# Kernel optimization log

Measured on AMD Instinct MI355X. Metric: run time of the kernel, lower is better.

Reference implementation:

```python
import jax, jax.numpy as jnp
import numpy as np

N = 50000      # nodes
E = 600000     # edges
IN = 128       # in_channels
HID = 128      # GCN hidden width (fixed in module)
H = 4          # TransformerConv heads
C = 32         # out_channels per head (heads*C = 128)


def _lin(k, fan_in, fan_out):
    return jax.random.normal(k, (fan_in, fan_out), jnp.float32) / np.sqrt(fan_in)


def setup_inputs() -> dict:
    key = jax.random.key(0)
    ks = jax.random.split(key, 12)
    return {
        "x": jax.random.normal(ks[0], (N, IN), jnp.float32),
        "edge_index": jax.random.randint(ks[1], (2, E), 0, N, dtype=jnp.int32),
        "W_gcn": _lin(ks[2], IN, HID),
        "b_gcn": jnp.zeros((HID,), jnp.float32),
        "Wq": _lin(ks[3], HID, H * C),
        "bq": jnp.zeros((H * C,), jnp.float32),
        "Wk": _lin(ks[4], HID, H * C),
        "bk": jnp.zeros((H * C,), jnp.float32),
        "Wv": _lin(ks[5], HID, H * C),
        "bv": jnp.zeros((H * C,), jnp.float32),
        "Ws": _lin(ks[6], HID, H * C),
        "bs": jnp.zeros((H * C,), jnp.float32),
    }


def reference(x, edge_index, W_gcn, b_gcn, Wq, bq, Wk, bk, Wv, bv, Ws, bs):
    n = x.shape[0]
    idt = edge_index.dtype

    # ---- GCNConv: x' = D^{-1/2}(A+I)D^{-1/2} x W + b, then ReLU ----
    h = x @ W_gcn                                   # [N, HID] linear first (PyG order)
    loop = jnp.arange(n, dtype=idt)
    src = jnp.concatenate([edge_index[0], loop])    # with self-loops
    tgt = jnp.concatenate([edge_index[1], loop])
    deg = jax.ops.segment_sum(jnp.ones(src.shape, h.dtype), tgt, num_segments=n)
    dinv = jnp.where(deg > 0, jax.lax.rsqrt(deg), 0.0)
    norm = dinv[src] * dinv[tgt]                    # [E+N]
    h = jax.ops.segment_sum(h[src] * norm[:, None], tgt, num_segments=n)
    h = jax.nn.relu(h + b_gcn)                      # [N, HID]

    # ---- TransformerConv (heads=4, concat=True, no self-loops added) ----
    s, t = edge_index[0], edge_index[1]
    q = (h @ Wq + bq).reshape(n, H, C)
    k = (h @ Wk + bk).reshape(n, H, C)
    v = (h @ Wv + bv).reshape(n, H, C)

    alpha = jnp.einsum('ehc,ehc->eh', q[t], k[s]) / np.sqrt(C)   # [E, H]
    m = jax.lax.stop_gradient(jax.ops.segment_max(alpha, t, num_segments=n))
    ea = jnp.exp(alpha - m[t])
    denom = jax.ops.segment_sum(ea, t, num_segments=n)           # [N, H]
    w = ea / jnp.where(denom[t] > 0, denom[t], 1.0)              # softmax per target node

    out = jax.ops.segment_sum(w[:, :, None] * v[s], t, num_segments=n)  # [N, H, C]
    out = out.reshape(n, H * C)

    # root/skip connection (lin_skip)
    return out + h @ Ws + bs
```

## Files before the change

kernel.cpp:

```cpp
#include <hip/hip_runtime.h>
#include <hip/hip_bf16.h>

typedef __attribute__((ext_vector_type(8))) short short8;
typedef __attribute__((ext_vector_type(4))) float floatx4;
typedef _Float16 half2v __attribute__((ext_vector_type(2)));

__device__ __forceinline__ float ld_f(const void* p, int f32, int i) {
  if (f32) return ((const float*)p)[i];
  unsigned short u = ((const unsigned short*)p)[i];
  return __uint_as_float(((unsigned)u) << 16);
}
__device__ __forceinline__ short ld_bf(const void* p, int f32, int i) {
  if (!f32) return ((const short*)p)[i];
  __hip_bfloat16 h = __float2bfloat16(((const float*)p)[i]);
  return *reinterpret_cast<short*>(&h);
}
__device__ __forceinline__ unsigned short f_to_bfu(float v) {
  __hip_bfloat16 h = __float2bfloat16(v);
  return *reinterpret_cast<unsigned short*>(&h);
}
__device__ __forceinline__ short f_to_h(float v) {
  _Float16 h = (_Float16)v;
  return *reinterpret_cast<short*>(&h);
}

__global__ void init_kernel(const unsigned short* __restrict__ xs, int* __restrict__ flag,
                            int* __restrict__ cnt, int N) {
  if (blockIdx.x == 0) {
    __shared__ int sbad;
    if (threadIdx.x == 0) sbad = 0;
    __syncthreads();
    int bad = 0;
    for (int j = 2 * threadIdx.x; j < 16384; j += 512) {
      unsigned e = (xs[j] >> 7) & 0xFF;
      if (e >= 0xF0) bad = 1;
    }
    if (bad) atomicOr(&sbad, 1);
    __syncthreads();
    if (threadIdx.x == 0) flag[0] = sbad;
    return;
  }
  int i = (blockIdx.x - 1) * blockDim.x + threadIdx.x;
  if (i < N) cnt[i] = 0;
}

__global__ void prep_hist(const void* bg, const void* bq, const void* bk, const void* bv,
                          const void* bs, const void* Wg, const void* Wq, const void* Wk,
                          const void* Wv, const void* Ws, const int* __restrict__ flag,
                          float* __restrict__ bgf, float* __restrict__ bias512,
                          short* __restrict__ WpG, short* __restrict__ WpQ,
                          const int* __restrict__ ei, int* __restrict__ cnt, int E, int Gp) {
  if ((int)blockIdx.x >= Gp) {
    int e = (blockIdx.x - Gp) * blockDim.x + threadIdx.x;
    if (e < E) atomicAdd(&cnt[ei[E + e]], 1);
    return;
  }
  int tid = blockIdx.x * blockDim.x + threadIdx.x;
  int f = *flag;
  if (tid < 128) { bgf[tid] = ld_f(bg, f, tid); return; }
  if (tid < 640) {
    int t = tid - 128;
    const void* b = (t < 128) ? bq : (t < 256) ? bk : (t < 384) ? bv : bs;
    bias512[t] = ld_f(b, f, t & 127);
    return;
  }
  if (tid < 640 + 2048) {
    int id = tid - 640;
    int lane = id & 63, kb = (id >> 6) & 3, tn = id >> 8;
    int k0 = kb * 32 + (lane >> 4) * 8;
    int n = tn * 16 + (lane & 15);
    short* dst = WpG + (size_t)id * 8;
#pragma unroll
    for (int j = 0; j < 8; ++j) dst[j] = ld_bf(Wg, f, (k0 + j) * 128 + n);
    return;
  }
  if (tid < 640 + 2048 + 8192) {
    int id = tid - 640 - 2048;
    int lane = id & 63, kb = (id >> 6) & 3, tn = id >> 8;
    int k0 = kb * 32 + (lane >> 4) * 8;
    int n = tn * 16 + (lane & 15);
    const void* W = (n < 128) ? Wq : (n < 256) ? Wk : (n < 384) ? Wv : Ws;
    int col = n & 127;
    short* dst = WpQ + (size_t)id * 8;
#pragma unroll
    for (int j = 0; j < 8; ++j) dst[j] = ld_bf(W, f, (k0 + j) * 128 + col);
  }
}

__global__ void scanA(const int* __restrict__ cnt, int* __restrict__ chunkscan,
                      int* __restrict__ partials, int N) {
  __shared__ int sh[1024];
  int t = threadIdx.x;
  int g = blockIdx.x * 1024 + t;
  int v = (g < N) ? cnt[g] : 0;
  sh[t] = v;
  __syncthreads();
  for (int o = 1; o < 1024; o <<= 1) {
    int add = (t >= o) ? sh[t - o] : 0;
    __syncthreads();
    sh[t] += add;
    __syncthreads();
  }
  if (g < N) chunkscan[g] = sh[t];
  if (t == 1023) partials[blockIdx.x] = sh[1023];
}

__global__ void scanB(int* __restrict__ partials, int nb) {
  if (threadIdx.x == 0) {
    int run = 0;
    for (int b = 0; b < nb; ++b) {
      int t = partials[b];
      partials[b] = run;
      run += t;
    }
  }
}

__global__ void scanC(const int* __restrict__ cnt, const int* __restrict__ chunkscan,
                      const int* __restrict__ partials, int* __restrict__ rowptr,
                      int* __restrict__ cursor, float* __restrict__ dinv, int N) {
  int g = blockIdx.x * blockDim.x + threadIdx.x;
  if (g == 0) rowptr[0] = 0;
  if (g >= N) return;
  int c = cnt[g];
  int inc = chunkscan[g] + partials[g >> 10];
  rowptr[g + 1] = inc;
  cursor[g] = inc - c;
  dinv[g] = rsqrtf((float)c + 1.0f);
}

__global__ void gemmh0_fill(const void* __restrict__ X, const int* __restrict__ flag,
                            const short* __restrict__ Bp, const float* __restrict__ dinv,
                            short* __restrict__ C, int M, const int* __restrict__ ei,
                            int* __restrict__ cursor, int* __restrict__ srcs, int E, int Gg) {
  if ((int)blockIdx.x >= Gg) {
    int e = (blockIdx.x - Gg) * blockDim.x + threadIdx.x;
    if (e < E) {
      int t = ei[E + e];
      int pos = atomicAdd(&cursor[t], 1);
      srcs[pos] = ei[e];
    }
    return;
  }
  int wv = (blockIdx.x * blockDim.x + threadIdx.x) >> 6;
  int lane = threadIdx.x & 63;
  int tilesM = (M + 15) >> 4;
  if (wv >= tilesM) return;
  int f = *flag;
  int tm = wv;
  int m = tm * 16 + (lane & 15);
  int mc = m < M ? m : M - 1;
  int quad = lane >> 4;
  short8 a[4];
  if (f) {
    const float* xr = (const float*)X + (size_t)mc * 128 + quad * 8;
#pragma unroll
    for (int kb = 0; kb < 4; ++kb)
#pragma unroll
      for (int j = 0; j < 8; ++j) a[kb][j] = (short)f_to_bfu(xr[kb * 32 + j]);
  } else {
    const short* xr = (const short*)X + (size_t)mc * 128 + quad * 8;
#pragma unroll
    for (int kb = 0; kb < 4; ++kb) a[kb] = *(const short8*)(xr + kb * 32);
  }
  floatx4 acc[8];
#pragma unroll
  for (int tn = 0; tn < 8; ++tn) acc[tn] = (floatx4){0.f, 0.f, 0.f, 0.f};
#pragma unroll
  for (int kb = 0; kb < 4; ++kb) {
#pragma unroll
    for (int tn = 0; tn < 8; ++tn) {
      short8 b8 = *(const short8*)(Bp + ((size_t)(tn * 4 + kb) * 64 + lane) * 8);
      acc[tn] = __builtin_amdgcn_mfma_f32_16x16x32_bf16(a[kb], b8, acc[tn], 0, 0, 0);
    }
  }
  int row0 = tm * 16 + quad * 4;
  int cl = lane & 15;
  float dsc[4];
#pragma unroll
  for (int r = 0; r < 4; ++r) dsc[r] = (row0 + r < M) ? dinv[row0 + r] : 0.f;
#pragma unroll
  for (int tn = 0; tn < 8; ++tn)
#pragma unroll
    for (int r = 0; r < 4; ++r)
      if (row0 + r < M)
        C[(size_t)(row0 + r) * 128 + tn * 16 + cl] = (short)f_to_bfu(acc[tn][r] * dsc[r]);
}

__global__ void gcn_gather(const int* __restrict__ rowptr, const int* __restrict__ srcs,
                           const float* __restrict__ dinv, const unsigned* __restrict__ h0,
                           const float* __restrict__ bgf, unsigned* __restrict__ hbf, int N) {
  int node = (int)((blockIdx.x * (long long)blockDim.x + threadIdx.x) >> 6);
  if (node >= N) return;
  int lane = threadIdx.x & 63;
  int beg = rowptr[node], end = rowptr[node + 1];
  float ax = 0.f, ay = 0.f;
  int i = beg;
  for (; i + 3 < end; i += 4) {
    int s0 = srcs[i], s1 = srcs[i + 1], s2 = srcs[i + 2], s3 = srcs[i + 3];
    unsigned w0 = h0[(size_t)s0 * 64 + lane];
    unsigned w1 = h0[(size_t)s1 * 64 + lane];
    unsigned w2 = h0[(size_t)s2 * 64 + lane];
    unsigned w3 = h0[(size_t)s3 * 64 + lane];
    ax += __uint_as_float(w0 << 16) + __uint_as_float(w1 << 16) +
          __uint_as_float(w2 << 16) + __uint_as_float(w3 << 16);
    ay += __uint_as_float(w0 & 0xFFFF0000u) + __uint_as_float(w1 & 0xFFFF0000u) +
          __uint_as_float(w2 & 0xFFFF0000u) + __uint_as_float(w3 & 0xFFFF0000u);
  }
  for (; i < end; ++i) {
    unsigned w = h0[(size_t)srcs[i] * 64 + lane];
    ax += __uint_as_float(w << 16);
    ay += __uint_as_float(w & 0xFFFF0000u);
  }
  float dt = dinv[node];
  unsigned hw = h0[(size_t)node * 64 + lane];
  float2 bb = ((const float2*)bgf)[lane];
  float vx = (ax + __uint_as_float(hw << 16)) * dt + bb.x;
  float vy = (ay + __uint_as_float(hw & 0xFFFF0000u)) * dt + bb.y;
  vx = vx > 0.f ? vx : 0.f;
  vy = vy > 0.f ? vy : 0.f;
  hbf[(size_t)node * 64 + lane] = (unsigned)f_to_bfu(vx) | ((unsigned)f_to_bfu(vy) << 16);
}

__global__ void gemm_qkvs(const short* __restrict__ A, const short* __restrict__ Bp,
                          const float* __restrict__ bias512, short* __restrict__ qb,
                          short* __restrict__ kb_, short* __restrict__ vb,
                          short* __restrict__ skipb, int M) {
  int wv = (blockIdx.x * blockDim.x + threadIdx.x) >> 6;
  int lane = threadIdx.x & 63;
  int tilesM = (M + 15) >> 4;
  if (wv >= tilesM * 4) return;
  int tng = wv & 3, tm = wv >> 2;
  int m = tm * 16 + (lane & 15);
  int mc = m < M ? m : M - 1;
  int quad = lane >> 4;
  const short* Arow = A + (size_t)mc * 128 + quad * 8;
  short8 a[4];
#pragma unroll
  for (int kb = 0; kb < 4; ++kb) a[kb] = *(const short8*)(Arow + kb * 32);
  floatx4 acc[8];
#pragma unroll
  for (int j = 0; j < 8; ++j) acc[j] = (floatx4){0.f, 0.f, 0.f, 0.f};
#pragma unroll
  for (int kb = 0; kb < 4; ++kb) {
#pragma unroll
    for (int j = 0; j < 8; ++j) {
      int tn = tng * 8 + j;
      short8 b8 = *(const short8*)(Bp + ((size_t)(tn * 4 + kb) * 64 + lane) * 8);
      acc[j] = __builtin_amdgcn_mfma_f32_16x16x32_bf16(a[kb], b8, acc[j], 0, 0, 0);
    }
  }
  int row0 = tm * 16 + quad * 4;
  int cl = lane & 15;
  short* o = (tng == 0) ? qb : (tng == 1) ? kb_ : (tng == 2) ? vb : skipb;
  bool ash = tng < 2;
#pragma unroll
  for (int j = 0; j < 8; ++j) {
    int cc = j * 16 + cl;
    float b = bias512[tng * 128 + cc];
#pragma unroll
    for (int r = 0; r < 4; ++r) {
      int row = row0 + r;
      if (row >= M) continue;
      float val = acc[j][r] + b;
      o[(size_t)row * 128 + cc] = ash ? f_to_h(val) : (short)f_to_bfu(val);
    }
  }
}

__device__ __forceinline__ float dotred(half2v q2, unsigned kw) {
  half2v k2 = *reinterpret_cast<half2v*>(&kw);
#if __has_builtin(__builtin_amdgcn_fdot2)
  float p = __builtin_amdgcn_fdot2(q2, k2, 0.f, false);
#else
  float p = (float)q2[0] * (float)k2[0] + (float)q2[1] * (float)k2[1];
#endif
  p += __shfl_xor(p, 1, 16);
  p += __shfl_xor(p, 2, 16);
  p += __shfl_xor(p, 4, 16);
  p += __shfl_xor(p, 8, 16);
  return p * 0.17677669529663687f;
}

__global__ void attn_fused(const int* __restrict__ rowptr, const int* __restrict__ srcs,
                           const unsigned* __restrict__ qb, const unsigned* __restrict__ kb,
                           const unsigned* __restrict__ vb, const unsigned* __restrict__ skipb,
                           float* __restrict__ out, int N) {
  int node = (int)((blockIdx.x * (long long)blockDim.x + threadIdx.x) >> 6);
  if (node >= N) return;
  int lane = threadIdx.x & 63;
  unsigned qw = qb[(size_t)node * 64 + lane];
  half2v q2 = *reinterpret_cast<half2v*>(&qw);
  int beg = rowptr[node], end = rowptr[node + 1];

  float denom = 0.f, ax = 0.f, ay = 0.f;
  int i = beg;
  for (; i + 3 < end; i += 4) {
    int s0 = srcs[i], s1 = srcs[i + 1], s2 = srcs[i + 2], s3 = srcs[i + 3];
    unsigned kw0 = kb[(size_t)s0 * 64 + lane];
    unsigned kw1 = kb[(size_t)s1 * 64 + lane];
    unsigned kw2 = kb[(size_t)s2 * 64 + lane];
    unsigned kw3 = kb[(size_t)s3 * 64 + lane];
    unsigned vw0 = vb[(size_t)s0 * 64 + lane];
    unsigned vw1 = vb[(size_t)s1 * 64 + lane];
    unsigned vw2 = vb[(size_t)s2 * 64 + lane];
    unsigned vw3 = vb[(size_t)s3 * 64 + lane];
    float e0 = __expf(dotred(q2, kw0));
    float e1 = __expf(dotred(q2, kw1));
    float e2 = __expf(dotred(q2, kw2));
    float e3 = __expf(dotred(q2, kw3));
    denom += e0 + e1 + e2 + e3;
    ax += e0 * __uint_as_float(vw0 << 16) + e1 * __uint_as_float(vw1 << 16) +
          e2 * __uint_as_float(vw2 << 16) + e3 * __uint_as_float(vw3 << 16);
    ay += e0 * __uint_as_float(vw0 & 0xFFFF0000u) + e1 * __uint_as_float(vw1 & 0xFFFF0000u) +
          e2 * __uint_as_float(vw2 & 0xFFFF0000u) + e3 * __uint_as_float(vw3 & 0xFFFF0000u);
  }
  for (; i < end; ++i) {
    int s = srcs[i];
    unsigned kw = kb[(size_t)s * 64 + lane];
    unsigned vw = vb[(size_t)s * 64 + lane];
    float ea = __expf(dotred(q2, kw));
    denom += ea;
    ax += ea * __uint_as_float(vw << 16);
    ay += ea * __uint_as_float(vw & 0xFFFF0000u);
  }
  float r = denom > 0.f ? 1.f / denom : 0.f;
  unsigned sw = skipb[(size_t)node * 64 + lane];
  float2 o;
  o.x = ax * r + __uint_as_float(sw << 16);
  o.y = ay * r + __uint_as_float(sw & 0xFFFF0000u);
  ((float2*)out)[(size_t)node * 64 + lane] = o;
}

extern "C" void kernel_launch(void* const* d_in, const int* in_sizes, int n_in,
                              void* d_out, int out_size, void* d_ws, size_t ws_size,
                              hipStream_t stream) {
  const void* x  = d_in[0];
  const int* ei  = (const int*)d_in[1];
  const void* Wg = d_in[2];
  const void* bg = d_in[3];
  const void* Wq = d_in[4];
  const void* bq = d_in[5];
  const void* Wk = d_in[6];
  const void* bk = d_in[7];
  const void* Wv = d_in[8];
  const void* bv = d_in[9];
  const void* Ws = d_in[10];
  const void* bs = d_in[11];
  float* out = (float*)d_out;

  const int N = in_sizes[0] / 128;
  const int E = in_sizes[1] / 2;
  int tilesM = (N + 15) / 16;
  int nscan = (N + 1023) / 1024;
  const int B = 256;

  char* ws = (char*)d_ws;
  size_t off = 0;
  auto carve = [&](size_t bytes) -> void* {
    void* p = ws + off;
    off += (bytes + 255) & ~(size_t)255;
    return p;
  };
  int* flag = (int*)carve(256);
  float* bias512 = (float*)carve(512 * 4);
  float* bgf = (float*)carve(128 * 4);
  float* dinv = (float*)carve((size_t)N * 4);
  int* cnt = (int*)carve((size_t)N * 4);
  int* rowptr = (int*)carve((size_t)(N + 1) * 4);
  int* cursor = (int*)carve((size_t)N * 4);
  int* chunkscan = (int*)carve((size_t)N * 4);
  int* partials = (int*)carve((size_t)(nscan + 1) * 4);
  int* srcs = (int*)carve((size_t)E * 4);
  short* WpG = (short*)carve((size_t)16384 * 2);
  short* WpQ = (short*)carve((size_t)65536 * 2);
  short* h0bf = (short*)carve((size_t)N * 128 * 2);
  short* hbf = (short*)carve((size_t)N * 128 * 2);
  short* qb = (short*)carve((size_t)N * 128 * 2);
  short* kb = (short*)carve((size_t)N * 128 * 2);
  short* vb = (short*)carve((size_t)N * 128 * 2);
  short* skipb = (short*)carve((size_t)N * 128 * 2);

  int Gp = (10880 + B - 1) / B;
  int Gh = (E + B - 1) / B;
  int Gg = (tilesM * 64 + B - 1) / B;
  int Gf = (E + B - 1) / B;

  init_kernel<<<1 + (N + B - 1) / B, B, 0, stream>>>((const unsigned short*)x, flag, cnt, N);
  prep_hist<<<Gp + Gh, B, 0, stream>>>(bg, bq, bk, bv, bs, Wg, Wq, Wk, Wv, Ws, flag,
                                       bgf, bias512, WpG, WpQ, ei, cnt, E, Gp);
  scanA<<<nscan, 1024, 0, stream>>>(cnt, chunkscan, partials, N);
  scanB<<<1, 64, 0, stream>>>(partials, nscan);
  scanC<<<(N + B - 1) / B, B, 0, stream>>>(cnt, chunkscan, partials, rowptr, cursor, dinv, N);
  gemmh0_fill<<<Gg + Gf, B, 0, stream>>>(x, flag, WpG, dinv, h0bf, N, ei, cursor, srcs, E, Gg);
  gcn_gather<<<(N + 3) / 4, B, 0, stream>>>(rowptr, srcs, dinv, (const unsigned*)h0bf, bgf,
                                            (unsigned*)hbf, N);
  gemm_qkvs<<<(tilesM * 4 + 3) / 4, B, 0, stream>>>(hbf, WpQ, bias512, qb, kb, vb, skipb, N);
  attn_fused<<<(N + 3) / 4, B, 0, stream>>>(rowptr, srcs, (const unsigned*)qb,
                                            (const unsigned*)kb, (const unsigned*)vb,
                                            (const unsigned*)skipb, out, N);
}
```

Baseline: 298.2 us.

## Interleave K/V rows and split edges across sub-wavefronts in gather kernels

Q/K/V/skip GEMM now writes K and V into one interleaved buffer (4 fp16 K values next to 4 bf16 V values per 16-byte chunk). The attention kernel can then fetch both with a single 16-byte load per edge, and each half-wavefront handles alternate edges with a cross-half shuffle reduction at the end. The GCN gather likewise processes four edges at once per wavefront using 16-byte loads per lane, then reduces across quarters. This aims to cut the number of memory transactions per edge and improve latency hiding. The cost is extra cross-lane shuffles, and the final write is done by only part of the lanes.

```diff
diff --git a/kernel.cpp b/kernel.cpp
--- a/kernel.cpp
+++ b/kernel.cpp
@@ -23,6 +23,8 @@
   _Float16 h = (_Float16)v;
   return *reinterpret_cast<short*>(&h);
 }
+__device__ __forceinline__ float bflo(unsigned w) { return __uint_as_float(w << 16); }
+__device__ __forceinline__ float bfhi(unsigned w) { return __uint_as_float(w & 0xFFFF0000u); }
 
 __global__ void init_kernel(const unsigned short* __restrict__ xs, int* __restrict__ flag,
                             int* __restrict__ cnt, int N) {
@@ -193,39 +195,76 @@
   int node = (int)((blockIdx.x * (long long)blockDim.x + threadIdx.x) >> 6);
   if (node >= N) return;
   int lane = threadIdx.x & 63;
+  int q = lane >> 4, sl = lane & 15;
   int beg = rowptr[node], end = rowptr[node + 1];
-  float ax = 0.f, ay = 0.f;
-  int i = beg;
-  for (; i + 3 < end; i += 4) {
-    int s0 = srcs[i], s1 = srcs[i + 1], s2 = srcs[i + 2], s3 = srcs[i + 3];
-    unsigned w0 = h0[(size_t)s0 * 64 + lane];
-    unsigned w1 = h0[(size_t)s1 * 64 + lane];
-    unsigned w2 = h0[(size_t)s2 * 64 + lane];
-    unsigned w3 = h0[(size_t)s3 * 64 + lane];
-    ax += __uint_as_float(w0 << 16) + __uint_as_float(w1 << 16) +
-          __uint_as_float(w2 << 16) + __uint_as_float(w3 << 16);
-    ay += __uint_as_float(w0 & 0xFFFF0000u) + __uint_as_float(w1 & 0xFFFF0000u) +
-          __uint_as_float(w2 & 0xFFFF0000u) + __uint_as_float(w3 & 0xFFFF0000u);
-  }
-  for (; i < end; ++i) {
-    unsigned w = h0[(size_t)srcs[i] * 64 + lane];
-    ax += __uint_as_float(w << 16);
-    ay += __uint_as_float(w & 0xFFFF0000u);
-  }
-  float dt = dinv[node];
-  unsigned hw = h0[(size_t)node * 64 + lane];
-  float2 bb = ((const float2*)bgf)[lane];
-  float vx = (ax + __uint_as_float(hw << 16)) * dt + bb.x;
-  float vy = (ay + __uint_as_float(hw & 0xFFFF0000u)) * dt + bb.y;
-  vx = vx > 0.f ? vx : 0.f;
-  vy = vy > 0.f ? vy : 0.f;
-  hbf[(size_t)node * 64 + lane] = (unsigned)f_to_bfu(vx) | ((unsigned)f_to_bfu(vy) << 16);
+  float a0 = 0.f, a1 = 0.f, a2 = 0.f, a3 = 0.f, a4 = 0.f, a5 = 0.f, a6 = 0.f, a7 = 0.f;
+  int i = beg + q;
+  for (; i + 4 < end; i += 8) {
+    int s0 = srcs[i], s1 = srcs[i + 4];
+    uint4 w0 = *(const uint4*)(h0 + (size_t)s0 * 64 + sl * 4);
+    uint4 w1 = *(const uint4*)(h0 + (size_t)s1 * 64 + sl * 4);
+    a0 += bflo(w0.x) + bflo(w1.x);
+    a1 += bfhi(w0.x) + bfhi(w1.x);
+    a2 += bflo(w0.y) + bflo(w1.y);
+    a3 += bfhi(w0.y) + bfhi(w1.y);
+    a4 += bflo(w0.z) + bflo(w1.z);
+    a5 += bfhi(w0.z) + bfhi(w1.z);
+    a6 += bflo(w0.w) + bflo(w1.w);
+    a7 += bfhi(w0.w) + bfhi(w1.w);
+  }
+  if (i < end) {
+    int s0 = srcs[i];
+    uint4 w0 = *(const uint4*)(h0 + (size_t)s0 * 64 + sl * 4);
+    a0 += bflo(w0.x);
+    a1 += bfhi(w0.x);
+    a2 += bflo(w0.y);
+    a3 += bfhi(w0.y);
+    a4 += bflo(w0.z);
+    a5 += bfhi(w0.z);
+    a6 += bflo(w0.w);
+    a7 += bfhi(w0.w);
+  }
+  a0 += __shfl_xor(a0, 16); a0 += __shfl_xor(a0, 32);
+  a1 += __shfl_xor(a1, 16); a1 += __shfl_xor(a1, 32);
+  a2 += __shfl_xor(a2, 16); a2 += __shfl_xor(a2, 32);
+  a3 += __shfl_xor(a3, 16); a3 += __shfl_xor(a3, 32);
+  a4 += __shfl_xor(a4, 16); a4 += __shfl_xor(a4, 32);
+  a5 += __shfl_xor(a5, 16); a5 += __shfl_xor(a5, 32);
+  a6 += __shfl_xor(a6, 16); a6 += __shfl_xor(a6, 32);
+  a7 += __shfl_xor(a7, 16); a7 += __shfl_xor(a7, 32);
+  if (q == 0) {
+    uint4 hw = *(const uint4*)(h0 + (size_t)node * 64 + sl * 4);
+    float dt = dinv[node];
+    const float4* bb = (const float4*)bgf;
+    float4 b0 = bb[sl * 2], b1 = bb[sl * 2 + 1];
+    float v0 = (a0 + bflo(hw.x)) * dt + b0.x;
+    float v1 = (a1 + bfhi(hw.x)) * dt + b0.y;
+    float v2 = (a2 + bflo(hw.y)) * dt + b0.z;
+    float v3 = (a3 + bfhi(hw.y)) * dt + b0.w;
+    float v4 = (a4 + bflo(hw.z)) * dt + b1.x;
+    float v5 = (a5 + bfhi(hw.z)) * dt + b1.y;
+    float v6 = (a6 + bflo(hw.w)) * dt + b1.z;
+    float v7 = (a7 + bfhi(hw.w)) * dt + b1.w;
+    v0 = v0 > 0.f ? v0 : 0.f;
+    v1 = v1 > 0.f ? v1 : 0.f;
+    v2 = v2 > 0.f ? v2 : 0.f;
+    v3 = v3 > 0.f ? v3 : 0.f;
+    v4 = v4 > 0.f ? v4 : 0.f;
+    v5 = v5 > 0.f ? v5 : 0.f;
+    v6 = v6 > 0.f ? v6 : 0.f;
+    v7 = v7 > 0.f ? v7 : 0.f;
+    uint4 o;
+    o.x = (unsigned)f_to_bfu(v0) | ((unsigned)f_to_bfu(v1) << 16);
+    o.y = (unsigned)f_to_bfu(v2) | ((unsigned)f_to_bfu(v3) << 16);
+    o.z = (unsigned)f_to_bfu(v4) | ((unsigned)f_to_bfu(v5) << 16);
+    o.w = (unsigned)f_to_bfu(v6) | ((unsigned)f_to_bfu(v7) << 16);
+    *(uint4*)(hbf + (size_t)node * 64 + sl * 4) = o;
+  }
 }
 
 __global__ void gemm_qkvs(const short* __restrict__ A, const short* __restrict__ Bp,
                           const float* __restrict__ bias512, short* __restrict__ qb,
-                          short* __restrict__ kb_, short* __restrict__ vb,
-                          short* __restrict__ skipb, int M) {
+                          short* __restrict__ kvb, short* __restrict__ skipb, int M) {
   int wv = (blockIdx.x * blockDim.x + threadIdx.x) >> 6;
   int lane = threadIdx.x & 63;
   int tilesM = (M + 15) >> 4;
@@ -252,8 +291,6 @@
   }
   int row0 = tm * 16 + quad * 4;
   int cl = lane & 15;
-  short* o = (tng == 0) ? qb : (tng == 1) ? kb_ : (tng == 2) ? vb : skipb;
-  bool ash = tng < 2;
 #pragma unroll
   for (int j = 0; j < 8; ++j) {
     int cc = j * 16 + cl;
@@ -263,73 +300,88 @@
       int row = row0 + r;
       if (row >= M) continue;
       float val = acc[j][r] + b;
-      o[(size_t)row * 128 + cc] = ash ? f_to_h(val) : (short)f_to_bfu(val);
-    }
-  }
-}
-
-__device__ __forceinline__ float dotred(half2v q2, unsigned kw) {
-  half2v k2 = *reinterpret_cast<half2v*>(&kw);
+      if (tng == 0) {
+        qb[(size_t)row * 128 + cc] = f_to_h(val);
+      } else if (tng == 3) {
+        skipb[(size_t)row * 128 + cc] = (short)f_to_bfu(val);
+      } else {
+        size_t base = (size_t)row * 256 + (size_t)((cc >> 2) * 8 + (cc & 3));
+        if (tng == 1)
+          kvb[base] = f_to_h(val);
+        else
+          kvb[base + 4] = (short)f_to_bfu(val);
+      }
+    }
+  }
+}
+
+__device__ __forceinline__ float dotred8(half2v qa, half2v qc, unsigned kw0, unsigned kw1) {
+  half2v k0 = *reinterpret_cast<half2v*>(&kw0);
+  half2v k1 = *reinterpret_cast<half2v*>(&kw1);
 #if __has_builtin(__builtin_amdgcn_fdot2)
-  float p = __builtin_amdgcn_fdot2(q2, k2, 0.f, false);
+  float p = __builtin_amdgcn_fdot2(qa, k0, 0.f, false);
+  p = __builtin_amdgcn_fdot2(qc, k1, p, false);
 #else
-  float p = (float)q2[0] * (float)k2[0] + (float)q2[1] * (float)k2[1];
+  float p = (float)qa[0] * (float)k0[0] + (float)qa[1] * (float)k0[1] +
+            (float)qc[0] * (float)k1[0] + (float)qc[1] * (float)k1[1];
 #endif
-  p += __shfl_xor(p, 1, 16);
-  p += __shfl_xor(p, 2, 16);
-  p += __shfl_xor(p, 4, 16);
-  p += __shfl_xor(p, 8, 16);
+  p += __shfl_xor(p, 1, 8);
+  p += __shfl_xor(p, 2, 8);
+  p += __shfl_xor(p, 4, 8);
   return p * 0.17677669529663687f;
 }
 
 __global__ void attn_fused(const int* __restrict__ rowptr, const int* __restrict__ srcs,
-                           const unsigned* __restrict__ qb, const unsigned* __restrict__ kb,
-                           const unsigned* __restrict__ vb, const unsigned* __restrict__ skipb,
-                           float* __restrict__ out, int N) {
+                           const unsigned* __restrict__ qb, const unsigned* __restrict__ kvb,
+                           const unsigned* __restrict__ skipb, float* __restrict__ out, int N) {
   int node = (int)((blockIdx.x * (long long)blockDim.x + threadIdx.x) >> 6);
   if (node >= N) return;
   int lane = threadIdx.x & 63;
-  unsigned qw = qb[(size_t)node * 64 + lane];
-  half2v q2 = *reinterpret_cast<half2v*>(&qw);
+  int hf = lane >> 5, sl = lane & 31;
+  uint2 qw = *(const uint2*)(qb + (size_t)node * 64 + sl * 2);
+  half2v qa = *reinterpret_cast<half2v*>(&qw.x);
+  half2v qc = *reinterpret_cast<half2v*>(&qw.y);
   int beg = rowptr[node], end = rowptr[node + 1];
 
-  float denom = 0.f, ax = 0.f, ay = 0.f;
-  int i = beg;
-  for (; i + 3 < end; i += 4) {
-    int s0 = srcs[i], s1 = srcs[i + 1], s2 = srcs[i + 2], s3 = srcs[i + 3];
-    unsigned kw0 = kb[(size_t)s0 * 64 + lane];
-    unsigned kw1 = kb[(size_t)s1 * 64 + lane];
-    unsigned kw2 = kb[(size_t)s2 * 64 + lane];
-    unsigned kw3 = kb[(size_t)s3 * 64 + lane];
-    unsigned vw0 = vb[(size_t)s0 * 64 + lane];
-    unsigned vw1 = vb[(size_t)s1 * 64 + lane];
-    unsigned vw2 = vb[(size_t)s2 * 64 + lane];
-    unsigned vw3 = vb[(size_t)s3 * 64 + lane];
-    float e0 = __expf(dotred(q2, kw0));
-    float e1 = __expf(dotred(q2, kw1));
-    float e2 = __expf(dotred(q2, kw2));
-    float e3 = __expf(dotred(q2, kw3));
-    denom += e0 + e1 + e2 + e3;
-    ax += e0 * __uint_as_float(vw0 << 16) + e1 * __uint_as_float(vw1 << 16) +
-          e2 * __uint_as_float(vw2 << 16) + e3 * __uint_as_float(vw3 << 16);
-    ay += e0 * __uint_as_float(vw0 & 0xFFFF0000u) + e1 * __uint_as_float(vw1 & 0xFFFF0000u) +
-          e2 * __uint_as_float(vw2 & 0xFFFF0000u) + e3 * __uint_as_float(vw3 & 0xFFFF0000u);
-  }
-  for (; i < end; ++i) {
-    int s = srcs[i];
-    unsigned kw = kb[(size_t)s * 64 + lane];
-    unsigned vw = vb[(size_t)s * 64 + lane];
-    float ea = __expf(dotred(q2, kw));
-    denom += ea;
-    ax += ea * __uint_as_float(vw << 16);
-    ay += ea * __uint_as_float(vw & 0xFFFF0000u);
-  }
-  float r = denom > 0.f ? 1.f / denom : 0.f;
-  unsigned sw = skipb[(size_t)node * 64 + lane];
-  float2 o;
-  o.x = ax * r + __uint_as_float(sw << 16);
-  o.y = ay * r + __uint_as_float(sw & 0xFFFF0000u);
-  ((float2*)out)[(size_t)node * 64 + lane] = o;
+  float denom = 0.f, ax0 = 0.f, ax1 = 0.f, ax2 = 0.f, ax3 = 0.f;
+  int i = beg + hf;
+  for (; i + 2 < end; i += 4) {
+    int s0 = srcs[i], s1 = srcs[i + 2];
+    uint4 kv0 = *(const uint4*)(kvb + (size_t)s0 * 128 + sl * 4);
+    uint4 kv1 = *(const uint4*)(kvb + (size_t)s1 * 128 + sl * 4);
+    float e0 = __expf(dotred8(qa, qc, kv0.x, kv0.y));
+    float e1 = __expf(dotred8(qa, qc, kv1.x, kv1.y));
+    denom += e0 + e1;
+    ax0 += e0 * bflo(kv0.z) + e1 * bflo(kv1.z);
+    ax1 += e0 * bfhi(kv0.z) + e1 * bfhi(kv1.z);
+    ax2 += e0 * bflo(kv0.w) + e1 * bflo(kv1.w);
+    ax3 += e0 * bfhi(kv0.w) + e1 * bfhi(kv1.w);
+  }
+  if (i < end) {
+    int s0 = srcs[i];
+    uint4 kv0 = *(const uint4*)(kvb + (size_t)s0 * 128 + sl * 4);
+    float e0 = __expf(dotred8(qa, qc, kv0.x, kv0.y));
+    denom += e0;
+    ax0 += e0 * bflo(kv0.z);
+    ax1 += e0 * bfhi(kv0.z);
+    ax2 += e0 * bflo(kv0.w);
+    ax3 += e0 * bfhi(kv0.w);
+  }
+  denom += __shfl_xor(denom, 32);
+  ax0 += __shfl_xor(ax0, 32);
+  ax1 += __shfl_xor(ax1, 32);
+  ax2 += __shfl_xor(ax2, 32);
+  ax3 += __shfl_xor(ax3, 32);
+  if (hf == 0) {
+    float r = denom > 0.f ? 1.f / denom : 0.f;
+    uint2 sw = *(const uint2*)(skipb + (size_t)node * 64 + sl * 2);
+    float4 o;
+    o.x = ax0 * r + bflo(sw.x);
+    o.y = ax1 * r + bfhi(sw.x);
+    o.z = ax2 * r + bflo(sw.y);
+    o.w = ax3 * r + bfhi(sw.y);
+    *(float4*)(out + (size_t)node * 128 + sl * 4) = o;
+  }
 }
 
 extern "C" void kernel_launch(void* const* d_in, const int* in_sizes, int n_in,
@@ -377,8 +429,7 @@
   short* h0bf = (short*)carve((size_t)N * 128 * 2);
   short* hbf = (short*)carve((size_t)N * 128 * 2);
   short* qb = (short*)carve((size_t)N * 128 * 2);
-  short* kb = (short*)carve((size_t)N * 128 * 2);
-  short* vb = (short*)carve((size_t)N * 128 * 2);
+  short* kvb = (short*)carve((size_t)N * 256 * 2);
   short* skipb = (short*)carve((size_t)N * 128 * 2);
 
   int Gp = (10880 + B - 1) / B;
@@ -395,8 +446,7 @@
   gemmh0_fill<<<Gg + Gf, B, 0, stream>>>(x, flag, WpG, dinv, h0bf, N, ei, cursor, srcs, E, Gg);
   gcn_gather<<<(N + 3) / 4, B, 0, stream>>>(rowptr, srcs, dinv, (const unsigned*)h0bf, bgf,
                                             (unsigned*)hbf, N);
-  gemm_qkvs<<<(tilesM * 4 + 3) / 4, B, 0, stream>>>(hbf, WpQ, bias512, qb, kb, vb, skipb, N);
+  gemm_qkvs<<<(tilesM * 4 + 3) / 4, B, 0, stream>>>(hbf, WpQ, bias512, qb, kvb, skipb, N);
   attn_fused<<<(N + 3) / 4, B, 0, stream>>>(rowptr, srcs, (const unsigned*)qb,
-                                            (const unsigned*)kb, (const unsigned*)vb,
-                                            (const unsigned*)skipb, out, N);
-}
+                                            (const unsigned*)kvb, (const unsigned*)skipb, out, N);
+}
```

Result: no change. 297.8 us (-0.1%).
